# Performance work log

Hardware: AMD Instinct MI355X
Metric: run time of the kernel (lower is better)

Reference implementation:

```python
import jax, jax.numpy as jnp
import numpy as np

VOCAB = 25
HIDDEN = 512
OUT = 1000
BATCH = 64
SEQ = 512


def setup_inputs() -> dict:
    key = jax.random.key(0)
    ks = jax.random.split(key, 12)
    s_in = 1.0 / np.sqrt(HIDDEN)  # torch nn.RNN init scale U(-1/sqrt(H), 1/sqrt(H))
    def u(k, shape):
        return jax.random.uniform(k, shape, jnp.float32, -s_in, s_in)
    return {
        "x": jax.random.randint(ks[0], (BATCH, SEQ), 0, VOCAB, dtype=jnp.int64),
        "W_ih0": u(ks[1], (HIDDEN, VOCAB)),
        "W_hh0": u(ks[2], (HIDDEN, HIDDEN)),
        "b_ih0": u(ks[3], (HIDDEN,)),
        "b_hh0": u(ks[4], (HIDDEN,)),
        "W_ih1": u(ks[5], (HIDDEN, HIDDEN)),
        "W_hh1": u(ks[6], (HIDDEN, HIDDEN)),
        "b_ih1": u(ks[7], (HIDDEN,)),
        "b_hh1": u(ks[8], (HIDDEN,)),
        "W_out": u(ks[9], (OUT, HIDDEN)),
        "b_out": u(ks[10], (OUT,)),
    }


def _rnn_scan(xw, W_hh, b_hh):
    # xw: [B, T, H] = precomputed x @ W_ih^T + b_ih. Scan the tanh recurrence.
    B, T, H = xw.shape
    def step(h, xt):
        h = jnp.tanh(xt + h @ W_hh.T + b_hh)
        return h, h
    h0 = jnp.zeros((B, H), xw.dtype)
    _, hs = jax.lax.scan(step, h0, jnp.swapaxes(xw, 0, 1))  # [T, B, H]
    return jnp.swapaxes(hs, 0, 1)  # [B, T, H]


def reference(x, W_ih0, W_hh0, b_ih0, b_hh0, W_ih1, W_hh1, b_ih1, b_hh1, W_out, b_out):
    # one_hot(x) @ W_ih0^T == gather of columns of W_ih0 -> same math, no dense matmul
    xw0 = jnp.take(W_ih0.T, x, axis=0) + b_ih0          # [B, T, H]
    h1 = _rnn_scan(xw0, W_hh0, b_hh0)                    # layer 0 outputs
    xw1 = jnp.einsum('bth,oh->bto', h1, W_ih1) + b_ih1   # [B, T, H]
    h2 = _rnn_scan(xw1, W_hh1, b_hh1)                    # layer 1 outputs
    last = h2[:, -1, :]                                  # [B, H]
    return last @ W_out.T + b_out                        # [B, OUT]
```

## Files before the change

### kernel.cpp

```cpp
#include <hip/hip_runtime.h>


#define HD 512
#define BATCH 64
#define SEQ 512
#define NVOCAB 25
#define OUTD 1000
#define BH (BATCH * HD)
#define BHQ (BH / 4)
#define IS64_OFF 2048
#define HDR_INTS 4096
#define GUARD_MAX (1L << 23)

typedef unsigned short u16;
typedef unsigned int u32;
typedef unsigned long long u64;
typedef __attribute__((ext_vector_type(8))) _Float16 half8;
typedef __attribute__((ext_vector_type(4))) u32 u32x4;
typedef __attribute__((ext_vector_type(4))) float f32x4;

union Frag16 { u32x4 x; u64 q[2]; u16 h[8]; half8 v; };

__device__ __forceinline__ u16 f2h(float f) {
    union { _Float16 h; u16 u; } c; c.h = (_Float16)f; return c.u;
}
__device__ __forceinline__ u64 ld64a(const u64* p) {
    return __hip_atomic_load((u64*)p, __ATOMIC_RELAXED, __HIP_MEMORY_SCOPE_AGENT);
}
__device__ __forceinline__ void st64a(u64* p, u64 v) {
    __hip_atomic_store(p, v, __ATOMIC_RELAXED, __HIP_MEMORY_SCOPE_AGENT);
}
#define LDX4(dst, addr) \
    asm volatile("global_load_dwordx4 %0, %1, off sc0" : "=v"(dst) : "v"(addr))
#define WAITV0() do { \
    asm volatile("s_waitcnt vmcnt(0)" ::: "memory"); \
    __builtin_amdgcn_sched_barrier(0); \
} while (0)

__device__ __forceinline__ u64 pack_tag(const u16 hv[4], u32 tag) {
    return ((u64)(((u32)hv[0] & 0xFFFEu) | tag))
         | ((u64)hv[1] << 16) | ((u64)hv[2] << 32) | ((u64)hv[3] << 48);
}

__device__ __forceinline__ float fast_tanh(float x) {
    float xc = fminf(fmaxf(x, -9.0f), 9.0f);
    float E = __expf(xc + xc);
    return __fdividef(E - 1.0f, E + 1.0f);
}

__global__ void init_kernel(int* hdr, u64* h1, u64* h2, const int* x32) {
    long i = (long)blockIdx.x * 256 + threadIdx.x;
    if (i < HDR_INTS) {
        if (i == IS64_OFF) {
            int all0 = 1;
            for (int j = 0; j < 64; ++j) if (x32[2 * j + 1] != 0) all0 = 0;
            hdr[i] = all0;
        } else hdr[i] = 0;
    } else {
        long r = i - HDR_INTS;
        if (r < 2L * BHQ) h1[r] = (r < BHQ) ? 0ull : 1ull;
        else if (r < 4L * BHQ) h2[r - 2L * BHQ] = 1ull;
    }
}

__global__ __launch_bounds__(64, 1) void rnn_fused(
    const float* __restrict__ Whh0, const float* __restrict__ Wih0,
    const int* __restrict__ x,
    const float* __restrict__ bih0, const float* __restrict__ bhh0,
    const float* __restrict__ Whh1, const float* __restrict__ Wih1,
    const float* __restrict__ bih1, const float* __restrict__ bhh1,
    u64* h1ring, u64* h2ring, float* h2final, int* hdr)
{
    const int lane = threadIdx.x & 63;
    const int quad = lane >> 4;
    const int l16  = lane & 15;
    const int u    = (int)blockIdx.x >> 2;
    const int cg   = (int)blockIdx.x & 3;
    const int rowbase = u * 16;
    const int arow = rowbase + l16;
    const int row0 = rowbase + quad * 4;
    const int col  = cg * 16 + l16;
    const int pg = lane & 31;
    const size_t repoff = (size_t)(cg * 16 + (pg & 15)) * 128 + pg * 4 + (pg & 3);

    half8 A0[16], A1[16], Aw[16];
    #pragma unroll
    for (int kc = 0; kc < 16; ++kc) {
        Frag16 t0, t1, tw;
        #pragma unroll
        for (int j = 0; j < 8; ++j) {
            const int widx = arow * HD + kc * 32 + quad * 8 + j;
            t0.h[j] = f2h(Whh0[widx]);
            t1.h[j] = f2h(Whh1[widx]);
            tw.h[j] = f2h(Wih1[widx]);
        }
        A0[kc] = t0.v; A1[kc] = t1.v; Aw[kc] = tw.v;
    }
    float bs0[4], bs1[4];
    #pragma unroll
    for (int i = 0; i < 4; ++i) {
        bs0[i] = bih0[row0 + i] + bhh0[row0 + i];
        bs1[i] = bih1[row0 + i] + bhh1[row0 + i];
    }
    const int is64 = hdr[IS64_OFF];

    long guard = 0;

    for (int t = 0; t <= SEQ; ++t) {
        const int tt = (t < SEQ) ? t : (SEQ - 1);
        int xi = is64 ? (int)((const long long*)x)[col * SEQ + tt]
                      : x[col * SEQ + tt];
        float wx[4];
        #pragma unroll
        for (int i = 0; i < 4; ++i) wx[i] = Wih0[(row0 + i) * NVOCAB + xi];

        const int rs = t & 1;
        const u32 e1 = (u32)((t >> 1) & 1);
        const u32 e2 = (u32)(((t + 2) >> 1) & 1);
        const u64* sb1 = h1ring + (size_t)rs * BHQ;
        const u64* sb2 = h2ring + (size_t)rs * BHQ;
        {
            const u64* rep = (lane < 32) ? (sb1 + repoff) : (sb2 + repoff);
            const u32 exr = (lane < 32) ? e1 : e2;
            for (;;) {
                u32 bad = (((u32)ld64a(rep)) ^ exr) & 1u;
                if (__ballot(bad != 0) == 0ULL) break;
                if (++guard > GUARD_MAX) break;
                __builtin_amdgcn_s_sleep(1);
            }
        }
        const u64* pb1 = sb1 + (size_t)col * 128 + quad * 2;
        const u64* pb2 = sb2 + (size_t)col * 128 + quad * 2;
        Frag16 B1[16], B2[16];
        for (;;) {
            #pragma unroll
            for (int kc = 0; kc < 16; ++kc) {
                LDX4(B1[kc].x, pb1 + kc * 8);
                LDX4(B2[kc].x, pb2 + kc * 8);
            }
            WAITV0();
            u32 bad = 0;
            #pragma unroll
            for (int kc = 0; kc < 16; ++kc) {
                bad |= ((((u32)B1[kc].q[0]) ^ e1) | (((u32)B1[kc].q[1]) ^ e1)) & 1u;
                bad |= ((((u32)B2[kc].q[0]) ^ e2) | (((u32)B2[kc].q[1]) ^ e2)) & 1u;
            }
            if (__ballot(bad != 0) == 0ULL) break;
            if (++guard > GUARD_MAX) break;
        }
        f32x4 aH0 = {0.f, 0.f, 0.f, 0.f}, aH1 = aH0;
        f32x4 aS0 = aH0, aS1 = aH0, aI0 = aH0, aI1 = aH0;
        #pragma unroll
        for (int kc = 0; kc < 16; kc += 2) {
            aH0 = __builtin_amdgcn_mfma_f32_16x16x32_f16(A0[kc],     B1[kc].v,     aH0, 0, 0, 0);
            aS0 = __builtin_amdgcn_mfma_f32_16x16x32_f16(A1[kc],     B2[kc].v,     aS0, 0, 0, 0);
            aI0 = __builtin_amdgcn_mfma_f32_16x16x32_f16(Aw[kc],     B1[kc].v,     aI0, 0, 0, 0);
            aH1 = __builtin_amdgcn_mfma_f32_16x16x32_f16(A0[kc + 1], B1[kc + 1].v, aH1, 0, 0, 0);
            aS1 = __builtin_amdgcn_mfma_f32_16x16x32_f16(A1[kc + 1], B2[kc + 1].v, aS1, 0, 0, 0);
            aI1 = __builtin_amdgcn_mfma_f32_16x16x32_f16(Aw[kc + 1], B1[kc + 1].v, aI1, 0, 0, 0);
        }
        float h0f[4], h1f[4]; u16 h0v[4], h1v[4];
        #pragma unroll
        for (int i = 0; i < 4; ++i) {
            h0f[i] = fast_tanh(aH0[i] + aH1[i] + bs0[i] + wx[i]);
            h0v[i] = f2h(h0f[i]);
            h1f[i] = fast_tanh(aS0[i] + aS1[i] + aI0[i] + aI1[i] + bs1[i]);
            h1v[i] = f2h(h1f[i]);
        }
        const int ws = (t + 1) & 1;
        const size_t po = (size_t)col * 128 + (row0 >> 2);
        if (t < SEQ) {
            st64a(h1ring + (size_t)ws * BHQ + po,
                  pack_tag(h0v, (u32)(((t + 1) >> 1) & 1)));
            if (t >= 1)
                st64a(h2ring + (size_t)ws * BHQ + po,
                      pack_tag(h1v, (u32)(((t + 3) >> 1) & 1)));
        } else {
            *(f32x4*)(h2final + col * HD + row0) = *(f32x4*)h1f;
        }
    }
}

__global__ __launch_bounds__(256) void out_kernel(
    const float* __restrict__ h2last, const float* __restrict__ Wout,
    const float* __restrict__ bout, float* __restrict__ out)
{
    int o = blockIdx.x * 256 + threadIdx.x;
    int b = blockIdx.y;
    if (o >= OUTD) return;
    const float* hrow = h2last + b * HD;
    const float* wrow = Wout + o * HD;
    float acc = 0.f;
    for (int k = 0; k < HD; k += 4) {
        float4 hv = *(const float4*)(hrow + k);
        float4 wv = *(const float4*)(wrow + k);
        acc += hv.x * wv.x + hv.y * wv.y + hv.z * wv.z + hv.w * wv.w;
    }
    out[b * OUTD + o] = acc + bout[o];
}

extern "C" void kernel_launch(void* const* d_in, const int* in_sizes, int n_in,
                              void* d_out, int out_size, void* d_ws, size_t ws_size,
                              hipStream_t stream) {
    const int*   x     = (const int*)d_in[0];
    const float* W_ih0 = (const float*)d_in[1];
    const float* W_hh0 = (const float*)d_in[2];
    const float* b_ih0 = (const float*)d_in[3];
    const float* b_hh0 = (const float*)d_in[4];
    const float* W_ih1 = (const float*)d_in[5];
    const float* W_hh1 = (const float*)d_in[6];
    const float* b_ih1 = (const float*)d_in[7];
    const float* b_hh1 = (const float*)d_in[8];
    const float* W_out = (const float*)d_in[9];
    const float* b_out = (const float*)d_in[10];

    const size_t needed = (size_t)HDR_INTS * 4 + 4ULL * BHQ * 8 + (size_t)BH * 4;
    if (ws_size < needed) return;

    int* hdr = (int*)d_ws;
    u64* h1ring = (u64*)((char*)d_ws + (size_t)HDR_INTS * 4);
    u64* h2ring = h1ring + 2ULL * BHQ;
    float* h2final = (float*)(h2ring + 2ULL * BHQ);

    const long ninit = HDR_INTS + 4L * BHQ;
    init_kernel<<<(int)((ninit + 255) / 256), 256, 0, stream>>>(hdr, h1ring, h2ring, x);
    rnn_fused<<<128, 64, 0, stream>>>(W_hh0, W_ih0, x, b_ih0, b_hh0,
                                      W_hh1, W_ih1, b_ih1, b_hh1,
                                      h1ring, h2ring, h2final, hdr);
    out_kernel<<<dim3(4, BATCH), 256, 0, stream>>>(h2final, W_out, b_out, (float*)d_out);
}
```

Baseline: 1.812 ms.

## Split layer-0 and layer-1 waits to publish h1 before waiting on h2

Each step of the persistent wavefront-pipelined RNN kernel now waits only for the layer-0 hidden state first. It computes the layer-0 MFMAs and tanh and stores the new h1 before waiting on the layer-1 ring. The Wih1 projection then runs before the h2 wait, and the layer-1 recurrence after it. The aim is to shorten the critical path of the layer-0 recurrence across the 128 blocks so other blocks see h1 sooner. The cost is two polling phases per step instead of one, which adds synchronisation overhead.

```diff
diff --git a/kernel.cpp b/kernel.cpp
--- a/kernel.cpp
+++ b/kernel.cpp
@@ -119,59 +119,86 @@
         const u32 e2 = (u32)(((t + 2) >> 1) & 1);
         const u64* sb1 = h1ring + (size_t)rs * BHQ;
         const u64* sb2 = h2ring + (size_t)rs * BHQ;
+        const int ws = (t + 1) & 1;
+        const size_t po = (size_t)col * 128 + (row0 >> 2);
+
         {
-            const u64* rep = (lane < 32) ? (sb1 + repoff) : (sb2 + repoff);
-            const u32 exr = (lane < 32) ? e1 : e2;
+            const u64* rep = sb1 + repoff;
             for (;;) {
-                u32 bad = (((u32)ld64a(rep)) ^ exr) & 1u;
+                u32 bad = (((u32)ld64a(rep)) ^ e1) & 1u;
                 if (__ballot(bad != 0) == 0ULL) break;
                 if (++guard > GUARD_MAX) break;
                 __builtin_amdgcn_s_sleep(1);
             }
         }
         const u64* pb1 = sb1 + (size_t)col * 128 + quad * 2;
-        const u64* pb2 = sb2 + (size_t)col * 128 + quad * 2;
-        Frag16 B1[16], B2[16];
+        Frag16 B1[16];
         for (;;) {
             #pragma unroll
-            for (int kc = 0; kc < 16; ++kc) {
-                LDX4(B1[kc].x, pb1 + kc * 8);
-                LDX4(B2[kc].x, pb2 + kc * 8);
-            }
+            for (int kc = 0; kc < 16; ++kc) LDX4(B1[kc].x, pb1 + kc * 8);
             WAITV0();
             u32 bad = 0;
             #pragma unroll
-            for (int kc = 0; kc < 16; ++kc) {
+            for (int kc = 0; kc < 16; ++kc)
                 bad |= ((((u32)B1[kc].q[0]) ^ e1) | (((u32)B1[kc].q[1]) ^ e1)) & 1u;
-                bad |= ((((u32)B2[kc].q[0]) ^ e2) | (((u32)B2[kc].q[1]) ^ e2)) & 1u;
-            }
             if (__ballot(bad != 0) == 0ULL) break;
             if (++guard > GUARD_MAX) break;
         }
         f32x4 aH0 = {0.f, 0.f, 0.f, 0.f}, aH1 = aH0;
-        f32x4 aS0 = aH0, aS1 = aH0, aI0 = aH0, aI1 = aH0;
         #pragma unroll
         for (int kc = 0; kc < 16; kc += 2) {
             aH0 = __builtin_amdgcn_mfma_f32_16x16x32_f16(A0[kc],     B1[kc].v,     aH0, 0, 0, 0);
+            aH1 = __builtin_amdgcn_mfma_f32_16x16x32_f16(A0[kc + 1], B1[kc + 1].v, aH1, 0, 0, 0);
+        }
+        if (t < SEQ) {
+            u16 h0v[4];
+            #pragma unroll
+            for (int i = 0; i < 4; ++i)
+                h0v[i] = f2h(fast_tanh(aH0[i] + aH1[i] + bs0[i] + wx[i]));
+            st64a(h1ring + (size_t)ws * BHQ + po,
+                  pack_tag(h0v, (u32)(((t + 1) >> 1) & 1)));
+        }
+        f32x4 aI0 = {0.f, 0.f, 0.f, 0.f}, aI1 = aI0;
+        #pragma unroll
+        for (int kc = 0; kc < 16; kc += 2) {
+            aI0 = __builtin_amdgcn_mfma_f32_16x16x32_f16(Aw[kc],     B1[kc].v,     aI0, 0, 0, 0);
+            aI1 = __builtin_amdgcn_mfma_f32_16x16x32_f16(Aw[kc + 1], B1[kc + 1].v, aI1, 0, 0, 0);
+        }
+        {
+            const u64* rep = sb2 + repoff;
+            for (;;) {
+                u32 bad = (((u32)ld64a(rep)) ^ e2) & 1u;
+                if (__ballot(bad != 0) == 0ULL) break;
+                if (++guard > GUARD_MAX) break;
+                __builtin_amdgcn_s_sleep(1);
+            }
+        }
+        const u64* pb2 = sb2 + (size_t)col * 128 + quad * 2;
+        Frag16 B2[16];
+        for (;;) {
+            #pragma unroll
+            for (int kc = 0; kc < 16; ++kc) LDX4(B2[kc].x, pb2 + kc * 8);
+            WAITV0();
+            u32 bad = 0;
+            #pragma unroll
+            for (int kc = 0; kc < 16; ++kc)
+                bad |= ((((u32)B2[kc].q[0]) ^ e2) | (((u32)B2[kc].q[1]) ^ e2)) & 1u;
+            if (__ballot(bad != 0) == 0ULL) break;
+            if (++guard > GUARD_MAX) break;
+        }
+        f32x4 aS0 = {0.f, 0.f, 0.f, 0.f}, aS1 = aS0;
+        #pragma unroll
+        for (int kc = 0; kc < 16; kc += 2) {
             aS0 = __builtin_amdgcn_mfma_f32_16x16x32_f16(A1[kc],     B2[kc].v,     aS0, 0, 0, 0);
-            aI0 = __builtin_amdgcn_mfma_f32_16x16x32_f16(Aw[kc],     B1[kc].v,     aI0, 0, 0, 0);
-            aH1 = __builtin_amdgcn_mfma_f32_16x16x32_f16(A0[kc + 1], B1[kc + 1].v, aH1, 0, 0, 0);
             aS1 = __builtin_amdgcn_mfma_f32_16x16x32_f16(A1[kc + 1], B2[kc + 1].v, aS1, 0, 0, 0);
-            aI1 = __builtin_amdgcn_mfma_f32_16x16x32_f16(Aw[kc + 1], B1[kc + 1].v, aI1, 0, 0, 0);
-        }
-        float h0f[4], h1f[4]; u16 h0v[4], h1v[4];
+        }
+        float h1f[4]; u16 h1v[4];
         #pragma unroll
         for (int i = 0; i < 4; ++i) {
-            h0f[i] = fast_tanh(aH0[i] + aH1[i] + bs0[i] + wx[i]);
-            h0v[i] = f2h(h0f[i]);
             h1f[i] = fast_tanh(aS0[i] + aS1[i] + aI0[i] + aI1[i] + bs1[i]);
             h1v[i] = f2h(h1f[i]);
         }
-        const int ws = (t + 1) & 1;
-        const size_t po = (size_t)col * 128 + (row0 >> 2);
         if (t < SEQ) {
-            st64a(h1ring + (size_t)ws * BHQ + po,
-                  pack_tag(h0v, (u32)(((t + 1) >> 1) & 1)));
             if (t >= 1)
                 st64a(h2ring + (size_t)ws * BHQ + po,
                       pack_tag(h1v, (u32)(((t + 3) >> 1) & 1)));
```

Measured after the change: 2.102 ms. +16.0%, slower.
